# Kernel tuning notes

Hardware: AMD Instinct MI355X
Metric: run time of the kernel (lower is better)

## Reference

```python
import jax, jax.numpy as jnp
import numpy as np

B, V = 256, 128000

def setup_inputs() -> dict:
    key = jax.random.key(0)
    k1, k2, k3 = jax.random.split(key, 3)
    logits = jax.random.normal(k1, (B, V), dtype=jnp.float32)
    temperatures = jax.random.uniform(k2, (B,), dtype=jnp.float32)
    top_ps = jax.random.uniform(k3, (B,), dtype=jnp.float32)
    return {"logits": logits, "temperatures": temperatures, "top_ps": top_ps}

def reference(logits, temperatures, top_ps):
    logits = logits.astype(jnp.float32)
    greedy_tokens = jnp.argmax(logits, axis=-1)
    t = temperatures[:, None]
    greedy_mask = t <= 1e-10                       # [B, 1]
    safe_t = jnp.maximum(t, 1e-5)
    probs = jax.nn.softmax(logits / safe_t, axis=-1)  # [B, V]
    # descending sort of probs with indices
    order = jnp.argsort(-probs, axis=-1)           # [B, V]
    sorted_probs = jnp.take_along_axis(probs, order, axis=-1)
    cum = jnp.cumsum(sorted_probs, axis=-1)
    mask = cum > top_ps[:, None]
    mask = mask.at[:, 0].set(False)                # always keep top-1
    sorted_probs = jnp.where(mask, 0.0, sorted_probs)
    # scatter the masked probs back to original vocab positions
    rows = jnp.arange(B)[:, None]
    probs = jnp.zeros_like(probs).at[rows, order].set(sorted_probs)
    probs = probs / jnp.sum(probs, axis=-1, keepdims=True)
    # Gumbel-max style sampling: argmax(probs / Exp(1) noise)
    noise = jax.random.exponential(jax.random.key(1), probs.shape, dtype=jnp.float32)
    noise = jnp.maximum(noise, 1e-10)
    sample_tokens = jnp.argmax(probs / noise, axis=-1)
    return jnp.where(greedy_mask[:, 0], greedy_tokens, sample_tokens)
```

## Files before the change

kernel.cpp:

```cpp
#include <hip/hip_runtime.h>
#include <stdint.h>

typedef unsigned long long u64;
typedef uint32_t u32;

#define BB 256
#define VV 128000
#define NV4 (VV / 4)
#define SLICES 16
#define SL4 (NV4 / SLICES)
#define NBUCK 4096
#define CAP 2048
#define QSCALE 1.099511627776e12f
#define QINV   (1.0 / 1099511627776.0)

#define OFF_SMAX 0
#define OFF_SARG (16*1024)
#define OFF_WWIN (32*1024)
#define OFF_PAR  (64*1024)
#define OFF_CNT  (72*1024)
#define OFF_HIST (80*1024)
#define OFF_LIST (OFF_HIST + (size_t)BB*NBUCK*8)
#define WS_TOTAL (OFF_LIST + (size_t)BB*CAP*8)

struct RowPar { int bstar; float thr; double M; double cutZ; };

#if defined(__has_builtin)
# if __has_builtin(__builtin_amdgcn_sched_barrier)
#  define SCHED_FENCE() __builtin_amdgcn_sched_barrier(0)
# endif
#endif
#ifndef SCHED_FENCE
# define SCHED_FENCE() asm volatile("" ::: "memory")
#endif

__device__ __forceinline__ u32 rotl32(u32 v, u32 r) { return (v << r) | (v >> (32u - r)); }

__device__ __forceinline__ u32 threefry_bits(u32 j) {
    const u32 ks0 = 0u, ks1 = 1u, ks2 = 0x1BD11BDBu;
    u32 x0 = ks0, x1 = j + ks1;
    x0 += x1; x1 = rotl32(x1, 13); x1 ^= x0;
    x0 += x1; x1 = rotl32(x1, 15); x1 ^= x0;
    x0 += x1; x1 = rotl32(x1, 26); x1 ^= x0;
    x0 += x1; x1 = rotl32(x1, 6);  x1 ^= x0;
    x0 += ks1; x1 += ks2 + 1u;
    x0 += x1; x1 = rotl32(x1, 17); x1 ^= x0;
    x0 += x1; x1 = rotl32(x1, 29); x1 ^= x0;
    x0 += x1; x1 = rotl32(x1, 16); x1 ^= x0;
    x0 += x1; x1 = rotl32(x1, 24); x1 ^= x0;
    x0 += ks2; x1 += ks0 + 2u;
    x0 += x1; x1 = rotl32(x1, 13); x1 ^= x0;
    x0 += x1; x1 = rotl32(x1, 15); x1 ^= x0;
    x0 += x1; x1 = rotl32(x1, 26); x1 ^= x0;
    x0 += x1; x1 = rotl32(x1, 6);  x1 ^= x0;
    x0 += ks0; x1 += ks1 + 3u;
    x0 += x1; x1 = rotl32(x1, 17); x1 ^= x0;
    x0 += x1; x1 = rotl32(x1, 29); x1 ^= x0;
    x0 += x1; x1 = rotl32(x1, 16); x1 ^= x0;
    x0 += x1; x1 = rotl32(x1, 24); x1 ^= x0;
    x0 += ks1; x1 += ks2 + 4u;
    x0 += x1; x1 = rotl32(x1, 13); x1 ^= x0;
    x0 += x1; x1 = rotl32(x1, 15); x1 ^= x0;
    x0 += x1; x1 = rotl32(x1, 26); x1 ^= x0;
    x0 += x1; x1 = rotl32(x1, 6);  x1 ^= x0;
    x0 += ks2; x1 += ks0 + 5u;
    return x0 ^ x1;
}

__device__ __forceinline__ float q_of(float x, float invT, float xm) {
    return __expf(fmaf(x, invT, -xm));
}

__device__ __forceinline__ float noise_of(u32 j) {
    u32 bits = threefry_bits(j);
    float u = __uint_as_float((bits >> 9) | 0x3F800000u) - 1.0f;
    return fmaxf(-log1pf(-u), 1e-10f);
}

extern "C" __global__ void __launch_bounds__(256, 1)
k1_stats(const float* __restrict__ logits, float* __restrict__ smax,
         int* __restrict__ sarg, u64* __restrict__ Whist, int* __restrict__ Wcnt) {
    int blk = blockIdx.x, r = blk >> 4, s = blk & 15;
    int tid = threadIdx.x, lane = tid & 63, wid = tid >> 6;
    __shared__ float sf[4]; __shared__ int si[4];
    Whist[(size_t)r * NBUCK + s * 256 + tid] = 0ULL;
    if (s == 0 && tid == 0) Wcnt[r] = 0;
    const float4* L4 = (const float4*)(logits + (size_t)r * VV);
    int i0 = s * SL4 + tid;
    bool h7 = tid < (SL4 - 7 * 256);
    float4 b0 = L4[i0],          b1 = L4[i0 + 256],  b2 = L4[i0 + 512];
    float4 b3 = L4[i0 + 768],    b4 = L4[i0 + 1024], b5 = L4[i0 + 1280];
    float4 b6 = L4[i0 + 1536],   b7 = L4[h7 ? i0 + 1792 : i0];
    SCHED_FENCE();
    float m = -3.402823466e38f; int mi = 0x7FFFFFFF;
    auto upd = [&](float4 a, int iv) {
        float m4 = fmaxf(fmaxf(a.x, a.y), fmaxf(a.z, a.w));
        if (m4 > m) {
            int base = iv * 4;
            if      (a.x == m4) mi = base;
            else if (a.y == m4) mi = base + 1;
            else if (a.z == m4) mi = base + 2;
            else                mi = base + 3;
            m = m4;
        }
    };
    upd(b0, i0);        upd(b1, i0 + 256);  upd(b2, i0 + 512);  upd(b3, i0 + 768);
    upd(b4, i0 + 1024); upd(b5, i0 + 1280); upd(b6, i0 + 1536);
    if (h7) upd(b7, i0 + 1792);
    for (int off = 32; off; off >>= 1) {
        float ov = __shfl_down(m, off); int oi = __shfl_down(mi, off);
        if (ov > m || (ov == m && oi < mi)) { m = ov; mi = oi; }
    }
    if (lane == 0) { sf[wid] = m; si[wid] = mi; }
    __syncthreads();
    if (tid == 0) {
        for (int w = 1; w < 4; w++) {
            float ov = sf[w]; int oi = si[w];
            if (ov > m || (ov == m && oi < mi)) { m = ov; mi = oi; }
        }
        smax[blk] = m; sarg[blk] = mi;
    }
}

extern "C" __global__ void __launch_bounds__(256, 1)
k2_hist(const float* __restrict__ logits, const float* __restrict__ smax,
        const float* __restrict__ temps, u64* __restrict__ Whist) {
    __shared__ u64 lh[NBUCK];
    int blk = blockIdx.x, r = blk >> 4, s = blk & 15, tid = threadIdx.x;
    for (int i = tid; i < NBUCK; i += 256) lh[i] = 0ULL;
    float T = fmaxf(temps[r], 1e-5f), invT = 1.0f / T;
    float rm = -3.402823466e38f;
    for (int j = 0; j < 16; j++) rm = fmaxf(rm, smax[r * 16 + j]);
    float xm = rm * invT;
    __syncthreads();
    const float4* L4 = (const float4*)(logits + (size_t)r * VV);
    int i0 = s * SL4 + tid;
    bool h7 = tid < (SL4 - 7 * 256);
    float4 b0 = L4[i0],          b1 = L4[i0 + 256],  b2 = L4[i0 + 512];
    float4 b3 = L4[i0 + 768],    b4 = L4[i0 + 1024], b5 = L4[i0 + 1280];
    float4 b6 = L4[i0 + 1536],   b7 = L4[h7 ? i0 + 1792 : i0];
    SCHED_FENCE();
    auto proc = [&](float4 x) {
        float xs[4] = {x.x, x.y, x.z, x.w};
        #pragma unroll
        for (int k = 0; k < 4; k++) {
            float t = fmaf(xs[k], invT, -xm);
            if (t < -104.0f) continue;
            float q = __expf(t);
            u32 pb = __float_as_uint(q);
            if (pb) atomicAdd(&lh[pb >> 18], (u64)(q * QSCALE));
        }
    };
    proc(b0); proc(b1); proc(b2); proc(b3); proc(b4); proc(b5); proc(b6);
    if (h7) proc(b7);
    __syncthreads();
    u64* gh = Whist + (size_t)r * NBUCK;
    for (int i = tid; i < NBUCK; i += 256) {
        u64 v = lh[i];
        if (v) atomicAdd(&gh[i], v);
    }
}

extern "C" __global__ void __launch_bounds__(1024)
k3_cut(const u64* __restrict__ Whist, const float* __restrict__ topps,
       RowPar* __restrict__ par) {
    int r = blockIdx.x, tid = threadIdx.x, lane = tid & 63, wid = tid >> 6;
    __shared__ double wtot[16];
    __shared__ double sh_cutZ; __shared__ int sh_b; __shared__ double sh_M;
    const u64* gh = Whist + (size_t)r * NBUCK;
    double h0 = (double)gh[4 * tid]     * QINV;
    double h1 = (double)gh[4 * tid + 1] * QINV;
    double h2 = (double)gh[4 * tid + 2] * QINV;
    double h3 = (double)gh[4 * tid + 3] * QINV;
    double s3 = h3, s2 = s3 + h2, s1 = s2 + h1, s0 = s1 + h0;
    double incl = s0;
    for (int off = 1; off < 64; off <<= 1) {
        double u = __shfl_down(incl, off);
        if (lane + off < 64) incl += u;
    }
    double excl = __shfl_down(incl, 1); if (lane == 63) excl = 0.0;
    if (lane == 0) wtot[wid] = incl;
    if (tid == 0) { sh_b = -1; sh_M = 0.0; }
    __syncthreads();
    double cw = 0.0;
    for (int w = wid + 1; w < 16; w++) cw += wtot[w];
    double carry = excl + cw;
    if (tid == 0) sh_cutZ = (double)topps[r] * (s0 + carry);
    __syncthreads();
    double cutZ = sh_cutZ;
    double S0 = s0 + carry, S1 = s1 + carry, S2 = s2 + carry, S3 = s3 + carry;
    if (S0 > cutZ && S1 <= cutZ)    { sh_b = 4 * tid;     sh_M = S1; }
    if (S1 > cutZ && S2 <= cutZ)    { sh_b = 4 * tid + 1; sh_M = S2; }
    if (S2 > cutZ && S3 <= cutZ)    { sh_b = 4 * tid + 2; sh_M = S3; }
    if (S3 > cutZ && carry <= cutZ) { sh_b = 4 * tid + 3; sh_M = carry; }
    __syncthreads();
    if (tid == 0) {
        float thr = -3.402823466e38f;
        if (sh_b > 0) {
            float qlo = __uint_as_float((u32)sh_b << 18);
            if (qlo >= 1.17549435e-38f) thr = logf(qlo) - 1e-3f;
        }
        RowPar p; p.bstar = sh_b; p.thr = thr; p.M = sh_M; p.cutZ = cutZ;
        par[r] = p;
    }
}

extern "C" __global__ void __launch_bounds__(256, 1)
k4_race(const float* __restrict__ logits, const float* __restrict__ smax,
        const float* __restrict__ temps, const RowPar* __restrict__ par,
        int* __restrict__ Wcnt, u64* __restrict__ Wlist, u64* __restrict__ Wwin) {
    int blk = blockIdx.x, r = blk >> 4, s = blk & 15;
    int tid = threadIdx.x, lane = tid & 63, wid = tid >> 6;
    __shared__ u64 wred[4];
    float T = fmaxf(temps[r], 1e-5f), invT = 1.0f / T;
    float rm = -3.402823466e38f;
    for (int j = 0; j < 16; j++) rm = fmaxf(rm, smax[r * 16 + j]);
    float xm = rm * invT;
    int bstar = par[r].bstar;
    float thr = par[r].thr;
    const float4* L4 = (const float4*)(logits + (size_t)r * VV);
    u32 jbase = (u32)r * (u32)VV;
    u64 pk = 0ULL;
    int i0 = s * SL4 + tid;
    bool h7 = tid < (SL4 - 7 * 256);
    float4 b0 = L4[i0],          b1 = L4[i0 + 256],  b2 = L4[i0 + 512];
    float4 b3 = L4[i0 + 768],    b4 = L4[i0 + 1024], b5 = L4[i0 + 1280];
    float4 b6 = L4[i0 + 1536],   b7 = L4[h7 ? i0 + 1792 : i0];
    SCHED_FENCE();
    auto proc = [&](float4 x, int iv) {
        float xs[4] = {x.x, x.y, x.z, x.w};
        int base = iv * 4;
        #pragma unroll
        for (int k = 0; k < 4; k++) {
            float t = fmaf(xs[k], invT, -xm);
            if (t < thr) continue;
            float q = __expf(t);
            u32 pb = __float_as_uint(q);
            if (!pb) continue;
            int b = (int)(pb >> 18);
            if (b > bstar) {
                u32 v = (u32)(base + k);
                float nz = noise_of(jbase + v);
                float sc = __fdividef(q, nz);
                u64 e = ((u64)__float_as_uint(sc) << 32) | (u64)(~v);
                if (e > pk) pk = e;
            } else if (b == bstar) {
                int pos = atomicAdd(&Wcnt[r], 1);
                if (pos < CAP)
                    Wlist[(size_t)r * CAP + pos] = ((u64)pb << 32) | (u64)(~(u32)(base + k));
            }
        }
    };
    proc(b0, i0);        proc(b1, i0 + 256);  proc(b2, i0 + 512);  proc(b3, i0 + 768);
    proc(b4, i0 + 1024); proc(b5, i0 + 1280); proc(b6, i0 + 1536);
    if (h7) proc(b7, i0 + 1792);
    for (int off = 32; off; off >>= 1) { u64 o = __shfl_down(pk, off); if (o > pk) pk = o; }
    if (lane == 0) wred[wid] = pk;
    __syncthreads();
    if (tid == 0) {
        for (int w = 1; w < 4; w++) if (wred[w] > pk) pk = wred[w];
        Wwin[blk] = pk;
    }
}

extern "C" __global__ void __launch_bounds__(1024)
k5_final(const float* __restrict__ smax, const int* __restrict__ sarg,
         const float* __restrict__ temps, const float* __restrict__ topps,
         const RowPar* __restrict__ par, const int* __restrict__ Wcnt,
         const u64* __restrict__ Wlist, const u64* __restrict__ Wwin,
         int* __restrict__ out) {
    int r = blockIdx.x, tid = threadIdx.x, lane = tid & 63, wid = tid >> 6;
    __shared__ u64 sb[CAP];
    __shared__ double wtot[16];
    __shared__ u64 wred[16];
    __shared__ int sh_js, sh_n, sh_gidx; __shared__ float sh_rm;
    RowPar p = par[r];
    if (tid == 0) {
        float rm = -3.402823466e38f; int gi = 0x7FFFFFFF;
        for (int j = 0; j < 16; j++) {
            float v = smax[r * 16 + j];
            if (v > rm) { rm = v; gi = sarg[r * 16 + j]; }
        }
        sh_rm = rm; sh_gidx = gi;
        int n = Wcnt[r]; if (n > CAP) n = CAP; sh_n = n;
        sh_js = 0x7FFFFFFF;
    }
    __syncthreads();
    int n = sh_n;
    int npad = 4; while (npad < n) npad <<= 1;
    const u64* lst = Wlist + (size_t)r * CAP;
    for (int i = tid; i < npad; i += 1024) sb[i] = (i < n) ? lst[i] : 0ULL;
    __syncthreads();
    for (int k = 2; k <= npad; k <<= 1) {
        for (int j = k >> 1; j > 0; j >>= 1) {
            for (int i = tid; i < npad; i += 1024) {
                int q2 = i ^ j;
                if (q2 > i) {
                    u64 a = sb[i], b = sb[q2];
                    bool desc = ((i & k) == 0);
                    if (desc ? (a < b) : (a > b)) { sb[i] = b; sb[q2] = a; }
                }
            }
            __syncthreads();
        }
    }
    int t2 = tid * 2;
    double f0 = 0.0, f1 = 0.0;
    if (t2 < npad) {
        f0 = (double)__uint_as_float((u32)(sb[t2] >> 32));
        f1 = (double)__uint_as_float((u32)(sb[t2 + 1] >> 32));
    }
    double c0 = f0, c1 = c0 + f1;
    double incl = c1;
    for (int off = 1; off < 64; off <<= 1) {
        double u = __shfl_up(incl, off);
        if (lane >= off) incl += u;
    }
    double excl = __shfl_up(incl, 1); if (lane == 0) excl = 0.0;
    double wt = __shfl(incl, 63);
    if (lane == 0) wtot[wid] = wt;
    __syncthreads();
    double cw = 0.0;
    for (int w = 0; w < wid; w++) cw += wtot[w];
    double cr = cw + excl;
    if (t2 < npad) {
        bool m0 = (p.M + (cr + c0)) > p.cutZ;
        bool m1 = (p.M + (cr + c1)) > p.cutZ;
        int cand = m0 ? t2 : m1 ? (t2 + 1) : 0x7FFFFFFF;
        if (cand != 0x7FFFFFFF) atomicMin(&sh_js, cand);
    }
    __syncthreads();
    float Traw = temps[r];
    if (tid == 0) {
        int js = sh_js; if (js > n) js = n;
        float T = fmaxf(Traw, 1e-5f), invT = 1.0f / T, xm = sh_rm * invT;
        int btop = (int)(__float_as_uint(q_of(sh_rm, invT, xm)) >> 18);
        if (js == 0 && p.bstar == btop) js = 1;
        sh_js = js;
    }
    __syncthreads();
    int js = sh_js;
    u32 jbase = (u32)r * (u32)VV;
    u64 pk = 0ULL;
    for (int i = tid; i < js; i += 1024) {
        u64 key = sb[i];
        float qq = __uint_as_float((u32)(key >> 32));
        u32 v = ~(u32)key;
        float nz = noise_of(jbase + v);
        float sc = __fdividef(qq, nz);
        u64 e = ((u64)__float_as_uint(sc) << 32) | (u64)(~v);
        if (e > pk) pk = e;
    }
    if (tid < 16) { u64 w = Wwin[r * 16 + tid]; if (w > pk) pk = w; }
    for (int off = 32; off; off >>= 1) { u64 o = __shfl_down(pk, off); if (o > pk) pk = o; }
    if (lane == 0) wred[wid] = pk;
    __syncthreads();
    if (tid == 0) {
        for (int w = 1; w < 16; w++) if (wred[w] > pk) pk = wred[w];
        int bi = (int)(~(u32)pk);
        out[r] = (Traw <= 1e-10f) ? sh_gidx : bi;
    }
}

extern "C" __global__ void __launch_bounds__(1024, 1)
sampler_fallback(const float* __restrict__ logits, const float* __restrict__ temps,
                 const float* __restrict__ topps, int* __restrict__ out)
{
    const int row = blockIdx.x;
    const int tid = threadIdx.x;
    const int lane = tid & 63;
    const int wid = tid >> 6;
    const float* L = logits + (size_t)row * VV;
    const float4* L4 = (const float4*)L;
    __shared__ __align__(16) unsigned char SMEM[32768];
    float* hist = (float*)SMEM;
    u64* sortbuf = (u64*)SMEM;
    __shared__ double wtot[16];
    __shared__ float wredf[16];
    __shared__ int wredi[16];
    __shared__ float sh_lmax;
    __shared__ int sh_gidx;
    __shared__ double sh_cutZ;
    __shared__ double sh_M;
    __shared__ int sh_bstar;
    __shared__ int sh_ng;
    __shared__ int sh_jstar;
    const float Traw = temps[row];
    const float T = fmaxf(Traw, 1e-5f);
    const float invT = 1.0f / T;
    const float tp = topps[row];
    float lmax = -3.402823466e38f; int lidx = 0x7FFFFFFF;
    for (int iv = tid; iv < NV4; iv += 1024) {
        float4 x = L4[iv];
        float m4 = fmaxf(fmaxf(x.x, x.y), fmaxf(x.z, x.w));
        if (m4 > lmax) {
            int base = iv * 4;
            if      (x.x == m4) lidx = base;
            else if (x.y == m4) lidx = base + 1;
            else if (x.z == m4) lidx = base + 2;
            else                lidx = base + 3;
            lmax = m4;
        }
    }
    for (int off = 32; off > 0; off >>= 1) {
        float ov = __shfl_down(lmax, off);
        int   oi = __shfl_down(lidx, off);
        if (ov > lmax || (ov == lmax && oi < lidx)) { lmax = ov; lidx = oi; }
    }
    if (lane == 0) { wredf[wid] = lmax; wredi[wid] = lidx; }
    for (int i = tid; i < NBUCK; i += 1024) hist[i] = 0.0f;
    __syncthreads();
    if (wid == 0) {
        float v = (lane < 16) ? wredf[lane] : -3.402823466e38f;
        int   i = (lane < 16) ? wredi[lane] : 0x7FFFFFFF;
        for (int off = 32; off > 0; off >>= 1) {
            float ov = __shfl_down(v, off);
            int   oi = __shfl_down(i, off);
            if (ov > v || (ov == v && oi < i)) { v = ov; i = oi; }
        }
        if (lane == 0) { sh_lmax = v; sh_gidx = i; }
    }
    __syncthreads();
    const float xm = sh_lmax * invT;
    const int gidx = sh_gidx;
    const int btop = (int)(__float_as_uint(q_of(sh_lmax, invT, xm)) >> 18);
    for (int iv = tid; iv < NV4; iv += 1024) {
        float4 x = L4[iv];
        float q0 = q_of(x.x, invT, xm), q1 = q_of(x.y, invT, xm);
        float q2 = q_of(x.z, invT, xm), q3 = q_of(x.w, invT, xm);
        u32 b0 = __float_as_uint(q0), b1 = __float_as_uint(q1);
        u32 b2 = __float_as_uint(q2), b3 = __float_as_uint(q3);
        if (b0) atomicAdd(&hist[b0 >> 18], q0);
        if (b1) atomicAdd(&hist[b1 >> 18], q1);
        if (b2) atomicAdd(&hist[b2 >> 18], q2);
        if (b3) atomicAdd(&hist[b3 >> 18], q3);
    }
    __syncthreads();
    float h0 = hist[4 * tid], h1 = hist[4 * tid + 1],
          h2 = hist[4 * tid + 2], h3 = hist[4 * tid + 3];
    double s3 = (double)h3, s2 = s3 + (double)h2, s1 = s2 + (double)h1, s0 = s1 + (double)h0;
    double incl = s0;
    for (int off = 1; off < 64; off <<= 1) {
        double u = __shfl_down(incl, off);
        if (lane + off < 64) incl += u;
    }
    double excl = __shfl_down(incl, 1);
    if (lane == 63) excl = 0.0;
    if (lane == 0) wtot[wid] = incl;
    __syncthreads();
    double cw = 0.0;
    for (int w = wid + 1; w < 16; w++) cw += wtot[w];
    const double carry = excl + cw;
    if (tid == 0) {
        sh_cutZ = (double)tp * (s0 + carry);
        sh_bstar = -1; sh_M = 0.0; sh_ng = 0; sh_jstar = 0x7FFFFFFF;
    }
    __syncthreads();
    const double cutZ = sh_cutZ;
    {
        double S0 = s0 + carry, S1 = s1 + carry, S2 = s2 + carry, S3 = s3 + carry;
        if (S0 > cutZ && S1 <= cutZ)    { sh_bstar = 4 * tid;     sh_M = S1; }
        if (S1 > cutZ && S2 <= cutZ)    { sh_bstar = 4 * tid + 1; sh_M = S2; }
        if (S2 > cutZ && S3 <= cutZ)    { sh_bstar = 4 * tid + 2; sh_M = S3; }
        if (S3 > cutZ && carry <= cutZ) { sh_bstar = 4 * tid + 3; sh_M = carry; }
    }
    __syncthreads();
    const int bstar = sh_bstar;
    const double M = sh_M;
    float bs = -1.0f; int bi = 0x7FFFFFFF;
    const u32 jbase = (u32)row * (u32)VV;
    for (int iv = tid; iv < NV4; iv += 1024) {
        float4 x = L4[iv];
        float qs[4] = {q_of(x.x, invT, xm), q_of(x.y, invT, xm),
                       q_of(x.z, invT, xm), q_of(x.w, invT, xm)};
        int base = iv * 4;
        #pragma unroll
        for (int k = 0; k < 4; k++) {
            u32 pb = __float_as_uint(qs[k]);
            if (pb == 0u) continue;
            int b = (int)(pb >> 18);
            if (b > bstar) {
                int v = base + k;
                float nz = noise_of(jbase + (u32)v);
                float sc = __fdividef(qs[k], nz);
                if (sc > bs || (sc == bs && v < bi)) { bs = sc; bi = v; }
            } else if (b == bstar) {
                int pos = atomicAdd(&sh_ng, 1);
                if (pos < 4096)
                    sortbuf[pos] = ((u64)pb << 32) | (u32)(~(u32)(base + k));
            }
        }
    }
    __syncthreads();
    if (bstar >= 0) {
        int n = sh_ng; if (n > 4096) n = 4096;
        int npad = 4; while (npad < n) npad <<= 1;
        for (int i = tid; i < npad; i += 1024) if (i >= n) sortbuf[i] = 0ULL;
        __syncthreads();
        for (int k = 2; k <= npad; k <<= 1) {
            for (int j = k >> 1; j > 0; j >>= 1) {
                for (int i = tid; i < npad; i += 1024) {
                    int pidx = i ^ j;
                    if (pidx > i) {
                        u64 a = sortbuf[i], b2 = sortbuf[pidx];
                        bool desc = ((i & k) == 0);
                        if (desc ? (a < b2) : (a > b2)) { sortbuf[i] = b2; sortbuf[pidx] = a; }
                    }
                }
                __syncthreads();
            }
        }
        double f0 = 0.0, f1 = 0.0, f2 = 0.0, f3 = 0.0;
        int t4 = tid * 4;
        if (t4 < npad) {
            f0 = (double)__uint_as_float((u32)(sortbuf[t4]     >> 32));
            f1 = (double)__uint_as_float((u32)(sortbuf[t4 + 1] >> 32));
            f2 = (double)__uint_as_float((u32)(sortbuf[t4 + 2] >> 32));
            f3 = (double)__uint_as_float((u32)(sortbuf[t4 + 3] >> 32));
        }
        double c0 = f0, c1 = c0 + f1, c2 = c1 + f2, c3 = c2 + f3;
        double incl2 = c3;
        for (int off = 1; off < 64; off <<= 1) {
            double u = __shfl_up(incl2, off);
            if (lane >= off) incl2 += u;
        }
        double excl2 = __shfl_up(incl2, 1);
        if (lane == 0) excl2 = 0.0;
        double wt = __shfl(incl2, 63);
        if (lane == 0) wtot[wid] = wt;
        __syncthreads();
        double cw2 = 0.0;
        for (int w = 0; w < wid; w++) cw2 += wtot[w];
        double cr = cw2 + excl2;
        if (t4 < npad) {
            bool m0 = (M + (cr + c0)) > cutZ;
            bool m1 = (M + (cr + c1)) > cutZ;
            bool m2 = (M + (cr + c2)) > cutZ;
            bool m3 = (M + (cr + c3)) > cutZ;
            int cand = m0 ? t4 : m1 ? (t4 + 1) : m2 ? (t4 + 2) : m3 ? (t4 + 3) : 0x7FFFFFFF;
            if (cand != 0x7FFFFFFF) atomicMin(&sh_jstar, cand);
        }
        __syncthreads();
        int jstar = sh_jstar; if (jstar > n) jstar = n;
        if (jstar == 0 && bstar == btop) jstar = 1;
        for (int i = tid; i < jstar; i += 1024) {
            u64 key = sortbuf[i];
            float qq = __uint_as_float((u32)(key >> 32));
            int v = (int)(~(u32)key);
            float nz = noise_of(jbase + (u32)v);
            float sc = __fdividef(qq, nz);
            if (sc > bs || (sc == bs && v < bi)) { bs = sc; bi = v; }
        }
    }
    for (int off = 32; off > 0; off >>= 1) {
        float ov = __shfl_down(bs, off);
        int   oi = __shfl_down(bi, off);
        if (ov > bs || (ov == bs && oi < bi)) { bs = ov; bi = oi; }
    }
    if (lane == 0) { wredf[wid] = bs; wredi[wid] = bi; }
    __syncthreads();
    if (tid == 0) {
        float v = wredf[0]; int i = wredi[0];
        for (int w = 1; w < 16; w++) {
            float ov = wredf[w]; int oi = wredi[w];
            if (ov > v || (ov == v && oi < i)) { v = ov; i = oi; }
        }
        out[row] = (Traw <= 1e-10f) ? gidx : i;
    }
}

extern "C" void kernel_launch(void* const* d_in, const int* in_sizes, int n_in,
                              void* d_out, int out_size, void* d_ws, size_t ws_size,
                              hipStream_t stream) {
    const float* logits = (const float*)d_in[0];
    const float* temps = (const float*)d_in[1];
    const float* topps = (const float*)d_in[2];
    int* out = (int*)d_out;
    (void)in_sizes; (void)n_in; (void)out_size;

    if (ws_size >= WS_TOTAL) {
        char* ws = (char*)d_ws;
        float* smax  = (float*)(ws + OFF_SMAX);
        int*   sarg  = (int*)(ws + OFF_SARG);
        u64*   wwin  = (u64*)(ws + OFF_WWIN);
        RowPar* par  = (RowPar*)(ws + OFF_PAR);
        int*   wcnt  = (int*)(ws + OFF_CNT);
        u64*   whist = (u64*)(ws + OFF_HIST);
        u64*   wlist = (u64*)(ws + OFF_LIST);
        k1_stats<<<BB * SLICES, 256, 0, stream>>>(logits, smax, sarg, whist, wcnt);
        k2_hist<<<BB * SLICES, 256, 0, stream>>>(logits, smax, temps, whist);
        k3_cut<<<BB, 1024, 0, stream>>>(whist, topps, par);
        k4_race<<<BB * SLICES, 256, 0, stream>>>(logits, smax, temps, par, wcnt, wlist, wwin);
        k5_final<<<BB, 1024, 0, stream>>>(smax, sarg, temps, topps, par, wcnt, wlist, wwin, out);
    } else {
        sampler_fallback<<<BB, 1024, 0, stream>>>(logits, temps, topps, out);
    }
}
```

Baseline: 388.7 us.

## Compact surviving candidates into LDS queues before noise evaluation in k4_race

```diff
diff --git a/kernel.cpp b/kernel.cpp
--- a/kernel.cpp
+++ b/kernel.cpp
@@ -211,7 +211,10 @@
         int* __restrict__ Wcnt, u64* __restrict__ Wlist, u64* __restrict__ Wwin) {
     int blk = blockIdx.x, r = blk >> 4, s = blk & 15;
     int tid = threadIdx.x, lane = tid & 63, wid = tid >> 6;
+    __shared__ u64 buf[2][1024];
+    __shared__ int qn[8];
     __shared__ u64 wred[4];
+    if (tid < 8) qn[tid] = 0;
     float T = fmaxf(temps[r], 1e-5f), invT = 1.0f / T;
     float rm = -3.402823466e38f;
     for (int j = 0; j < 16; j++) rm = fmaxf(rm, smax[r * 16 + j]);
@@ -227,33 +230,76 @@
     float4 b3 = L4[i0 + 768],    b4 = L4[i0 + 1024], b5 = L4[i0 + 1280];
     float4 b6 = L4[i0 + 1536],   b7 = L4[h7 ? i0 + 1792 : i0];
     SCHED_FENCE();
-    auto proc = [&](float4 x, int iv) {
-        float xs[4] = {x.x, x.y, x.z, x.w};
-        int base = iv * 4;
-        #pragma unroll
-        for (int k = 0; k < 4; k++) {
-            float t = fmaf(xs[k], invT, -xm);
-            if (t < thr) continue;
-            float q = __expf(t);
-            u32 pb = __float_as_uint(q);
-            if (!pb) continue;
-            int b = (int)(pb >> 18);
-            if (b > bstar) {
-                u32 v = (u32)(base + k);
-                float nz = noise_of(jbase + v);
-                float sc = __fdividef(q, nz);
-                u64 e = ((u64)__float_as_uint(sc) << 32) | (u64)(~v);
-                if (e > pk) pk = e;
-            } else if (b == bstar) {
-                int pos = atomicAdd(&Wcnt[r], 1);
-                if (pos < CAP)
-                    Wlist[(size_t)r * CAP + pos] = ((u64)pb << 32) | (u64)(~(u32)(base + k));
-            }
-        }
-    };
-    proc(b0, i0);        proc(b1, i0 + 256);  proc(b2, i0 + 512);  proc(b3, i0 + 768);
-    proc(b4, i0 + 1024); proc(b5, i0 + 1280); proc(b6, i0 + 1536);
-    if (h7) proc(b7, i0 + 1792);
+
+    #define K4_FILTER(c, VXV, off, valid) do {                                     \
+        float tt0 = fmaf((VXV).x, invT, -xm), tt1 = fmaf((VXV).y, invT, -xm);      \
+        float tt2 = fmaf((VXV).z, invT, -xm), tt3 = fmaf((VXV).w, invT, -xm);      \
+        int fbase = (i0 + (off)) * 4;                                              \
+        float fq0 = __expf(tt0), fq1 = __expf(tt1);                                \
+        float fq2 = __expf(tt2), fq3 = __expf(tt3);                                \
+        float fqs[4] = {fq0, fq1, fq2, fq3};                                       \
+        float fts[4] = {tt0, tt1, tt2, tt3};                                       \
+        _Pragma("unroll")                                                          \
+        for (int k = 0; k < 4; k++) {                                              \
+            u32 pb = __float_as_uint(fqs[k]);                                      \
+            bool pass = (valid) && (fts[k] >= thr) && (pb != 0u);                  \
+            u64 bm = __ballot(pass);                                               \
+            if (bm) {                                            \
+                int cnt = __popcll(bm);                                            \
+                int wb = 0;                                                        \
+                if (lane == 0) wb = atomicAdd(&qn[c], cnt);                        \
+                wb = __shfl(wb, 0);                                                \
+                if (pass) {                                                        \
+                    int o2 = __popcll(bm & ((1ULL << lane) - 1ULL));               \
+                    buf[(c) & 1][wb + o2] = ((u64)pb << 32) | (u32)(fbase + k);    \
+                }                                                                  \
+            }                                                                      \
+        }                                                                          \
+    } while (0)
+
+    #define K4_DENSE(c) do {                                                       \
+        int dn = qn[c];                                                            \
+        for (int di = tid; di < dn; di += 256) {                                   \
+            u64 de = buf[(c) & 1][di];                                             \
+            u32 pb = (u32)(de >> 32);                                              \
+            u32 dv = (u32)de;                                                      \
+            int db = (int)(pb >> 18);                                              \
+            if (db > bstar) {                                                      \
+                float dq = __uint_as_float(pb);                                    \
+                float nz = noise_of(jbase + dv);                                   \
+                float sc = __fdividef(dq, nz);                                     \
+                u64 ee = ((u64)__float_as_uint(sc) << 32) | (u64)(~dv);            \
+                if (ee > pk) pk = ee;                                              \
+            } else if (db == bstar) {                                              \
+                int pos = atomicAdd(&Wcnt[r], 1);                                  \
+                if (pos < CAP)                                                     \
+                    Wlist[(size_t)r * CAP + pos] = ((u64)pb << 32) | (u64)(~dv);   \
+            }                                                                      \
+        }                                                                          \
+    } while (0)
+
+    __syncthreads();
+    K4_FILTER(0, b0, 0, true);
+    __syncthreads();
+    K4_FILTER(1, b1, 256, true);   K4_DENSE(0);
+    __syncthreads();
+    K4_FILTER(2, b2, 512, true);   K4_DENSE(1);
+    __syncthreads();
+    K4_FILTER(3, b3, 768, true);   K4_DENSE(2);
+    __syncthreads();
+    K4_FILTER(4, b4, 1024, true);  K4_DENSE(3);
+    __syncthreads();
+    K4_FILTER(5, b5, 1280, true);  K4_DENSE(4);
+    __syncthreads();
+    K4_FILTER(6, b6, 1536, true);  K4_DENSE(5);
+    __syncthreads();
+    K4_FILTER(7, b7, 1792, h7);    K4_DENSE(6);
+    __syncthreads();
+    K4_DENSE(7);
+
+    #undef K4_FILTER
+    #undef K4_DENSE
+
     for (int off = 32; off; off >>= 1) { u64 o = __shfl_down(pk, off); if (o > pk) pk = o; }
     if (lane == 0) wred[wid] = pk;
     __syncthreads();
```

After: 349.9 us. 10.0% less time.
